# Kernel optimization log

Measured on AMD Instinct MI355X. Metric: run time of the kernel, lower is better.

Reference implementation:

```python
import jax, jax.numpy as jnp
import numpy as np
from jax import lax

T, B, F = 512, 256, 258
IN, H = 256, 1024


def setup_inputs() -> dict:
    key = jax.random.key(0)
    ks = jax.random.split(key, 6)

    def lin_w(k, fi, fo):
        return jax.random.normal(k, (fi, fo), jnp.float32) * (1.0 / np.sqrt(fi))

    return {
        "u": jax.random.normal(ks[0], (T, B, F), jnp.float32),
        "a": jnp.float32(0.92),
        "b": jnp.float32(-0.3),
        "W0": lin_w(ks[1], IN, H), "b0": jnp.zeros((H,), jnp.float32),
        "W1": lin_w(ks[2], H, H), "b1": jnp.zeros((H,), jnp.float32),
        "W2": lin_w(ks[3], H, H), "b2": jnp.zeros((H,), jnp.float32),
        "W3": lin_w(ks[4], H, 1), "b3": jnp.zeros((1,), jnp.float32),
    }


def reference(u, a, b, W0, b0, W1, b1, W2, b2, W3, b3):
    Tn, Bn, Fn = u.shape
    # MLP over cols 2: — independent of the recurrent state, so batch all timesteps.
    feats = u[:, :, 2:].reshape(Tn * Bn, Fn - 2)
    h = jax.nn.relu(feats @ W0 + b0)
    h = jax.nn.relu(h @ W1 + b1)
    h = jax.nn.relu(h @ W2 + b2)
    net = (h @ W3 + b3).reshape(Tn, Bn)  # [T, B]

    c1 = u[:, :, 1]  # [T, B], multiplied by b each step
    y0 = u[0, :, 0]  # u_y[0]; also the col-0 value used at j=0

    def step(carry, xs):
        net_j, c1_j = xs
        y = a * carry + b * c1_j + net_j
        return y, y

    _, ys = lax.scan(step, y0, (net, c1))  # ys: [T, B] = u_y[1:]
    return jnp.concatenate([y0[None, :], ys], axis=0)  # [T+1, B]
```

## Files before the change

### kernel.cpp

```cpp
#include <hip/hip_runtime.h>
#include <hip/hip_fp16.h>

typedef _Float16 v8h __attribute__((ext_vector_type(8)));
typedef _Float16 v4h __attribute__((ext_vector_type(4)));
typedef float v4f __attribute__((ext_vector_type(4)));

#define T_DIM 512
#define B_DIM 256
#define F_DIM 258
#define IN_DIM 256
#define H_DIM 1024
#define M_ROWS (T_DIM * B_DIM)

__device__ __forceinline__ void tile_map(int b, int nM, int nN, int& mt, int& nt) {
    if ((nM & 7) == 0) {
        int xcd = b & 7;
        int l = b >> 3;
        int mpx = nM >> 3;
        int lm = l / nN;
        mt = xcd * mpx + lm;
        nt = l - lm * nN;
    } else {
        int lm = b / nN;
        mt = lm;
        nt = b - lm * nN;
    }
}

__device__ __forceinline__ void gl16(const _Float16* g, _Float16* l) {
    __builtin_amdgcn_global_load_lds(
        (const __attribute__((address_space(1))) unsigned int*)g,
        (__attribute__((address_space(3))) unsigned int*)l, 16, 0, 0);
}


__global__ void prep_u_kernel(const float* __restrict__ u,
                              _Float16* __restrict__ X,
                              float* __restrict__ c1, int n) {
    int i = blockIdx.x * blockDim.x + threadIdx.x;
    int stride = gridDim.x * blockDim.x;
    for (; i < n; i += stride) {
        float v = u[i];
        unsigned r = (unsigned)i / 258u;
        unsigned c = (unsigned)i - r * 258u;
        if (c >= 2u) {
            unsigned k = c - 2u;
            X[((r >> 4) * 32u + (k >> 3)) * 128u + (r & 15u) * 8u + (k & 7u)] =
                (_Float16)v;
        } else if (c == 1u) {
            c1[r] = v;
        }
    }
}

__global__ void wt_frag_kernel(const float* __restrict__ W,
                               _Float16* __restrict__ BF, int K, int N) {
    int idx = blockIdx.x * blockDim.x + threadIdx.x;
    int total = (N >> 6) * (K >> 5) * 4 * 64;
    if (idx >= total) return;
    int l = idx & 63;
    int f = idx >> 6;
    int i = f & 3;
    int gk = f >> 2;
    int KC = K >> 5;
    int g = gk / KC, kc = gk - g * KC;
    int col = g * 64 + i * 16 + (l & 15);
    int krow = kc * 32 + (l >> 4) * 8;
    _Float16 tmp[8];
#pragma unroll
    for (int j = 0; j < 8; ++j) tmp[j] = (_Float16)W[(size_t)(krow + j) * N + col];
    *(v8h*)&BF[(size_t)idx * 8] = *(v8h*)tmp;
}

__global__ void wt_vec_kernel(const float* __restrict__ W,
                              _Float16* __restrict__ Wh, int K) {
    int i = blockIdx.x * blockDim.x + threadIdx.x;
    if (i < K) Wh[i] = (_Float16)W[i];
}

__global__ void zero_kernel(float* __restrict__ p, int n) {
    int i = blockIdx.x * blockDim.x + threadIdx.x;
    if (i < n) p[i] = 0.f;
}

template <int MI0>
__device__ __forceinline__ void mfma_pair(v4f (&acc)[8][4], const v8h (&af)[4][2],
                                          const v8h (&b)[4]) {
#pragma unroll
    for (int ni = 0; ni < 4; ++ni) {
        acc[MI0][ni] = __builtin_amdgcn_mfma_f32_16x16x32_f16(
            af[ni][0], b[0], acc[MI0][ni], 0, 0, 0);
        acc[MI0][ni] = __builtin_amdgcn_mfma_f32_16x16x32_f16(
            af[ni][1], b[1], acc[MI0][ni], 0, 0, 0);
        acc[MI0 + 1][ni] = __builtin_amdgcn_mfma_f32_16x16x32_f16(
            af[ni][0], b[2], acc[MI0 + 1][ni], 0, 0, 0);
        acc[MI0 + 1][ni] = __builtin_amdgcn_mfma_f32_16x16x32_f16(
            af[ni][1], b[3], acc[MI0 + 1][ni], 0, 0, 0);
    }
}

template <int DOT>
__global__ __launch_bounds__(512, 2)
void gemm256(const _Float16* __restrict__ Xb, const _Float16* __restrict__ WF,
             const float* __restrict__ bias, const _Float16* __restrict__ w3,
             _Float16* __restrict__ Cb, float* __restrict__ net,
             int M, int N, int K) {
    extern __shared__ _Float16 lds[];
    const int tid = threadIdx.x;
    const int lane = tid & 63;
    const int wave = tid >> 6;
    const int wm = wave >> 2;
    const int wn = wave & 3;
    const int quad = lane >> 4;
    const int r16 = lane & 15;
    const int wm8 = wm * 8;
    const int lrb = lane * 8;

    int mt, nt;
    tile_map(blockIdx.x, M >> 8, N >> 8, mt, nt);
    const int m0 = mt * 256;
    const int n0 = nt * 256;

    const int KC = K >> 5;
    const int KC8 = K >> 3;
    const int NT = K >> 6;
    const int m016 = m0 >> 4;
    const int nt4 = nt * 4;

    auto stageB = [&](int mb, int kt, _Float16* pb) {
        gl16(Xb + ((size_t)(m016 + mb + (tid >> 7)) * KC8 + (size_t)kt * 8) * 128 +
                 (tid & 127) * 8,
             pb + mb * 1024 + tid * 8);
    };
    auto loadB = [&](const _Float16* pB, int mb, v8h (&b)[4]) {
        b[0] = *(const v8h*)(pB + mb * 1024 + lrb);
        b[1] = *(const v8h*)(pB + mb * 1024 + 512 + lrb);
        b[2] = *(const v8h*)(pB + (mb + 1) * 1024 + lrb);
        b[3] = *(const v8h*)(pB + (mb + 1) * 1024 + 512 + lrb);
    };

    const _Float16* wp0 = WF + (size_t)(nt4 + wn) * KC * 2048 + lane * 8;

    v4f acc[8][4];
#pragma unroll
    for (int i = 0; i < 8; ++i)
#pragma unroll
        for (int j = 0; j < 4; ++j) acc[i][j] = (v4f)0.f;

    {
        stageB(0, 0, lds); stageB(4, 0, lds);
        stageB(8, 0, lds); stageB(12, 0, lds);
        asm volatile("s_waitcnt vmcnt(0)" ::: "memory");
        __builtin_amdgcn_s_barrier();
    }

#pragma unroll 2
    for (int kt = 0; kt < NT; ++kt) {
        _Float16* pBc = lds + (kt & 1) * 16384;
        _Float16* pBn = lds + ((kt + 1) & 1) * 16384;
        const bool pre = (kt + 1 < NT);
        const int kn = kt + 1;

        const _Float16* wpt = wp0 + (size_t)kt * 4096;
        v8h af[4][2];
#pragma unroll
        for (int i = 0; i < 4; ++i) {
            af[i][0] = *(const v8h*)(wpt + i * 512);
            af[i][1] = *(const v8h*)(wpt + 2048 + i * 512);
        }
        v8h bA[4], bB[4];
        loadB(pBc, wm8 + 0, bA);

        if (pre) {
            stageB(0, kn, pBn); stageB(4, kn, pBn);
            stageB(8, kn, pBn); stageB(12, kn, pBn);
        }

        loadB(pBc, wm8 + 2, bB);
        __builtin_amdgcn_s_setprio(1);
        mfma_pair<0>(acc, af, bA);
        __builtin_amdgcn_s_setprio(0);

        loadB(pBc, wm8 + 4, bA);
        __builtin_amdgcn_s_setprio(1);
        mfma_pair<2>(acc, af, bB);
        __builtin_amdgcn_s_setprio(0);

        loadB(pBc, wm8 + 6, bB);
        __builtin_amdgcn_s_setprio(1);
        mfma_pair<4>(acc, af, bA);
        __builtin_amdgcn_s_setprio(0);

        __builtin_amdgcn_s_setprio(1);
        mfma_pair<6>(acc, af, bB);
        __builtin_amdgcn_s_setprio(0);

        if (kt != NT - 1) {
            asm volatile("s_waitcnt lgkmcnt(0)" ::: "memory");
            asm volatile("s_waitcnt vmcnt(0)" ::: "memory");
            __builtin_amdgcn_s_barrier();
        }
    }

    const int nb = n0 + wn * 64;
    v4f bv[4];
#pragma unroll
    for (int ni = 0; ni < 4; ++ni)
        bv[ni] = *(const v4f*)&bias[nb + ni * 16 + quad * 4];

    if constexpr (DOT == 0) {
        const int NC8 = N >> 3;
#pragma unroll
        for (int ni = 0; ni < 4; ++ni) {
            const int nblk = ((nb + ni * 16) >> 3) + (quad >> 1);
#pragma unroll
            for (int mi = 0; mi < 8; ++mi) {
                v4h hv;
#pragma unroll
                for (int i = 0; i < 4; ++i)
                    hv[i] = (_Float16)fmaxf(acc[mi][ni][i] + bv[ni][i], 0.f);
                const size_t mblk = (size_t)((m0 + wm * 128 + mi * 16) >> 4);
                _Float16* dst =
                    Cb + (mblk * NC8 + nblk) * 128 + r16 * 8 + (quad & 1) * 4;
                *(v4h*)dst = hv;
            }
        }
    } else {
        v4h wv[4];
#pragma unroll
        for (int ni = 0; ni < 4; ++ni)
            wv[ni] = *(const v4h*)&w3[nb + ni * 16 + quad * 4];
#pragma unroll
        for (int mi = 0; mi < 8; ++mi) {
            float t = 0.f;
#pragma unroll
            for (int ni = 0; ni < 4; ++ni)
#pragma unroll
                for (int i = 0; i < 4; ++i) {
                    float v = fmaxf(acc[mi][ni][i] + bv[ni][i], 0.f);
                    t = fmaf(v, (float)wv[ni][i], t);
                }
            t += __shfl_xor(t, 16);
            t += __shfl_xor(t, 32);
            if (quad == 0) {
                int row = m0 + wm * 128 + mi * 16 + r16;
                atomicAdd(&net[row], t);
            }
        }
    }
}

__global__ void scan_kernel(const float* __restrict__ net,
                            const float* __restrict__ c1,
                            const float* __restrict__ u,
                            const float* __restrict__ pa,
                            const float* __restrict__ pb,
                            const float* __restrict__ pb3,
                            float* __restrict__ out) {
    const int bidx = threadIdx.x;
    const float a = pa[0];
    const float b = pb[0];
    const float b3 = pb3[0];
    float y = u[(size_t)bidx * F_DIM];
    out[bidx] = y;
#pragma unroll 8
    for (int t = 0; t < T_DIM; ++t) {
        float z = fmaf(b, c1[t * B_DIM + bidx], net[t * B_DIM + bidx] + b3);
        y = fmaf(a, y, z);
        out[(t + 1) * B_DIM + bidx] = y;
    }
}

extern "C" void kernel_launch(void* const* d_in, const int* in_sizes, int n_in,
                              void* d_out, int out_size, void* d_ws, size_t ws_size,
                              hipStream_t stream) {
    const float* u = (const float*)d_in[0];
    const float* pa = (const float*)d_in[1];
    const float* pb = (const float*)d_in[2];
    const float* W0 = (const float*)d_in[3];
    const float* b0 = (const float*)d_in[4];
    const float* W1 = (const float*)d_in[5];
    const float* b1 = (const float*)d_in[6];
    const float* W2 = (const float*)d_in[7];
    const float* b2 = (const float*)d_in[8];
    const float* W3 = (const float*)d_in[9];
    const float* b3 = (const float*)d_in[10];
    float* out = (float*)d_out;

    char* ws = (char*)d_ws;
    size_t off = 0;
    auto alloc = [&](size_t bytes) -> void* {
        void* p = ws + off;
        off += (bytes + 255) & ~(size_t)255;
        return p;
    };

    float* net = (float*)alloc((size_t)M_ROWS * 4);
    float* c1 = (float*)alloc((size_t)M_ROWS * 4);
    _Float16* W0F = (_Float16*)alloc((size_t)IN_DIM * H_DIM * 2);
    _Float16* W1F = (_Float16*)alloc((size_t)H_DIM * H_DIM * 2);
    _Float16* W2F = (_Float16*)alloc((size_t)H_DIM * H_DIM * 2);
    _Float16* W3h = (_Float16*)alloc((size_t)H_DIM * 2);

    const size_t per_row = 512 + 2048 + 2048;
    size_t avail = (ws_size > off + 65536) ? (ws_size - off - 65536) : 0;
    long Rl = (long)(avail / per_row);
    Rl = (Rl / 2048) * 2048;
    if (Rl < 2048) Rl = 2048;
    if (Rl > M_ROWS) Rl = M_ROWS;
    const int R = (int)Rl;

    _Float16* Xc = (_Float16*)alloc((size_t)R * IN_DIM * 2);
    _Float16* HAc = (_Float16*)alloc((size_t)R * H_DIM * 2);
    _Float16* HBc = (_Float16*)alloc((size_t)R * H_DIM * 2);

    wt_frag_kernel<<<(IN_DIM / 32) * (H_DIM / 64), 256, 0, stream>>>(W0, W0F,
                                                                     IN_DIM, H_DIM);
    wt_frag_kernel<<<(H_DIM / 32) * (H_DIM / 64), 256, 0, stream>>>(W1, W1F,
                                                                    H_DIM, H_DIM);
    wt_frag_kernel<<<(H_DIM / 32) * (H_DIM / 64), 256, 0, stream>>>(W2, W2F,
                                                                    H_DIM, H_DIM);
    wt_vec_kernel<<<4, 256, 0, stream>>>(W3, W3h, H_DIM);
    zero_kernel<<<M_ROWS / 256, 256, 0, stream>>>(net, M_ROWS);

    const size_t lds_bytes = 65536;
    for (int r0 = 0; r0 < M_ROWS; r0 += R) {
        int Mc = M_ROWS - r0;
        if (Mc > R) Mc = R;
        int nElem = Mc * F_DIM;
        int pgrid = (nElem + 256 * 8 - 1) / (256 * 8);
        if (pgrid > 2048) pgrid = 2048;
        prep_u_kernel<<<pgrid, 256, 0, stream>>>(u + (size_t)r0 * F_DIM, Xc,
                                                 c1 + r0, nElem);

        dim3 blk(512);
        dim3 grd((Mc / 256) * (H_DIM / 256));
        gemm256<0><<<grd, blk, lds_bytes, stream>>>(Xc, W0F, b0, nullptr, HAc,
                                                    nullptr, Mc, H_DIM, IN_DIM);
        gemm256<0><<<grd, blk, lds_bytes, stream>>>(HAc, W1F, b1, nullptr, HBc,
                                                    nullptr, Mc, H_DIM, H_DIM);
        gemm256<1><<<grd, blk, lds_bytes, stream>>>(HBc, W2F, b2, W3h, nullptr,
                                                    net + r0, Mc, H_DIM, H_DIM);
    }

    scan_kernel<<<1, 256, 0, stream>>>(net, c1, u, pa, pb, b3, out);
}
```

Baseline: 1.024 ms.

## Retile MLP GEMMs to 256x128 with LDS-staged weights and vectorize input prep

The GEMM block changes from 512 threads on a 256x256 tile with a 64-wide K step to 256 threads on a 256x128 tile with a 32-wide K step. Weight fragments are now staged into double-buffered LDS with global_load_lds instead of being read per wave straight from global memory, and LDS use drops to 48KB. The input prep kernel is split so the X conversion runs as 8-wide vectorized loads and stores without per-element division, while c1 gets its own small kernel. The smaller tile lowers arithmetic intensity and needs twice as many barriers per unit of K, in exchange for more blocks and less duplicated weight traffic.

```diff
diff --git a/kernel.cpp b/kernel.cpp
--- a/kernel.cpp
+++ b/kernel.cpp
@@ -34,23 +34,27 @@
 }
 
 
-__global__ void prep_u_kernel(const float* __restrict__ u,
-                              _Float16* __restrict__ X,
-                              float* __restrict__ c1, int n) {
+__global__ void prep_x_kernel(const float* __restrict__ u,
+                              _Float16* __restrict__ X, int nrows) {
     int i = blockIdx.x * blockDim.x + threadIdx.x;
+    int total = nrows * 32;
     int stride = gridDim.x * blockDim.x;
-    for (; i < n; i += stride) {
-        float v = u[i];
-        unsigned r = (unsigned)i / 258u;
-        unsigned c = (unsigned)i - r * 258u;
-        if (c >= 2u) {
-            unsigned k = c - 2u;
-            X[((r >> 4) * 32u + (k >> 3)) * 128u + (r & 15u) * 8u + (k & 7u)] =
-                (_Float16)v;
-        } else if (c == 1u) {
-            c1[r] = v;
-        }
-    }
+    for (; i < total; i += stride) {
+        int r = ((i >> 9) << 4) + (i & 15);
+        int kb = (i >> 4) & 31;
+        const float* s = u + (size_t)r * 258 + 2 + kb * 8;
+        _Float16 h[8];
+#pragma unroll
+        for (int j = 0; j < 8; ++j) h[j] = (_Float16)s[j];
+        *(v8h*)(X + ((size_t)(r >> 4) * 32 + kb) * 128 + (r & 15) * 8) =
+            *(v8h*)h;
+    }
+}
+
+__global__ void prep_c1_kernel(const float* __restrict__ u,
+                               float* __restrict__ c1, int nrows) {
+    int r = blockIdx.x * blockDim.x + threadIdx.x;
+    if (r < nrows) c1[r] = u[(size_t)r * 258 + 1];
 }
 
 __global__ void wt_frag_kernel(const float* __restrict__ W,
@@ -84,23 +88,18 @@
 }
 
 template <int MI0>
-__device__ __forceinline__ void mfma_pair(v4f (&acc)[8][4], const v8h (&af)[4][2],
-                                          const v8h (&b)[4]) {
-#pragma unroll
-    for (int ni = 0; ni < 4; ++ni) {
-        acc[MI0][ni] = __builtin_amdgcn_mfma_f32_16x16x32_f16(
-            af[ni][0], b[0], acc[MI0][ni], 0, 0, 0);
-        acc[MI0][ni] = __builtin_amdgcn_mfma_f32_16x16x32_f16(
-            af[ni][1], b[1], acc[MI0][ni], 0, 0, 0);
-        acc[MI0 + 1][ni] = __builtin_amdgcn_mfma_f32_16x16x32_f16(
-            af[ni][0], b[2], acc[MI0 + 1][ni], 0, 0, 0);
-        acc[MI0 + 1][ni] = __builtin_amdgcn_mfma_f32_16x16x32_f16(
-            af[ni][1], b[3], acc[MI0 + 1][ni], 0, 0, 0);
-    }
+__device__ __forceinline__ void mfma16(v4f (&acc)[8][4], const v8h (&af)[4],
+                                       const v8h (&b)[4]) {
+#pragma unroll
+    for (int mi = 0; mi < 4; ++mi)
+#pragma unroll
+        for (int ni = 0; ni < 4; ++ni)
+            acc[MI0 + mi][ni] = __builtin_amdgcn_mfma_f32_16x16x32_f16(
+                af[ni], b[mi], acc[MI0 + mi][ni], 0, 0, 0);
 }
 
 template <int DOT>
-__global__ __launch_bounds__(512, 2)
+__global__ __launch_bounds__(256, 2)
 void gemm256(const _Float16* __restrict__ Xb, const _Float16* __restrict__ WF,
              const float* __restrict__ bias, const _Float16* __restrict__ w3,
              _Float16* __restrict__ Cb, float* __restrict__ net,
@@ -109,38 +108,39 @@
     const int tid = threadIdx.x;
     const int lane = tid & 63;
     const int wave = tid >> 6;
-    const int wm = wave >> 2;
-    const int wn = wave & 3;
+    const int wm = wave >> 1;
+    const int wn = wave & 1;
     const int quad = lane >> 4;
     const int r16 = lane & 15;
     const int wm8 = wm * 8;
     const int lrb = lane * 8;
 
     int mt, nt;
-    tile_map(blockIdx.x, M >> 8, N >> 8, mt, nt);
+    tile_map(blockIdx.x, M >> 8, N >> 7, mt, nt);
     const int m0 = mt * 256;
-    const int n0 = nt * 256;
+    const int n0 = nt * 128;
 
     const int KC = K >> 5;
     const int KC8 = K >> 3;
-    const int NT = K >> 6;
+    const int NT = KC;
     const int m016 = m0 >> 4;
-    const int nt4 = nt * 4;
-
+    const int nt2 = nt * 2;
+
+    auto stageA = [&](int g, int kt, _Float16* pa) {
+        gl16(WF + ((size_t)(nt2 + g) * KC + kt) * 2048 + tid * 8,
+             pa + g * 2048 + tid * 8);
+    };
     auto stageB = [&](int mb, int kt, _Float16* pb) {
-        gl16(Xb + ((size_t)(m016 + mb + (tid >> 7)) * KC8 + (size_t)kt * 8) * 128 +
-                 (tid & 127) * 8,
-             pb + mb * 1024 + tid * 8);
+        gl16(Xb + ((size_t)(m016 + mb + (tid >> 6)) * KC8 + (size_t)kt * 4) * 128 +
+                 (tid & 63) * 8,
+             pb + mb * 512 + tid * 8);
     };
-    auto loadB = [&](const _Float16* pB, int mb, v8h (&b)[4]) {
-        b[0] = *(const v8h*)(pB + mb * 1024 + lrb);
-        b[1] = *(const v8h*)(pB + mb * 1024 + 512 + lrb);
-        b[2] = *(const v8h*)(pB + (mb + 1) * 1024 + lrb);
-        b[3] = *(const v8h*)(pB + (mb + 1) * 1024 + 512 + lrb);
+    auto loadB4 = [&](const _Float16* pB, int mb, v8h (&b)[4]) {
+#pragma unroll
+        for (int j = 0; j < 4; ++j)
+            b[j] = *(const v8h*)(pB + (mb + j) * 512 + lrb);
     };
 
-    const _Float16* wp0 = WF + (size_t)(nt4 + wn) * KC * 2048 + lane * 8;
-
     v4f acc[8][4];
 #pragma unroll
     for (int i = 0; i < 8; ++i)
@@ -148,55 +148,46 @@
         for (int j = 0; j < 4; ++j) acc[i][j] = (v4f)0.f;
 
     {
-        stageB(0, 0, lds); stageB(4, 0, lds);
-        stageB(8, 0, lds); stageB(12, 0, lds);
+        _Float16* A0 = lds;
+        _Float16* B0 = lds + 4096;
+        stageB(0, 0, B0); stageB(4, 0, B0); stageB(8, 0, B0); stageB(12, 0, B0);
+        stageA(0, 0, A0); stageA(1, 0, A0);
         asm volatile("s_waitcnt vmcnt(0)" ::: "memory");
         __builtin_amdgcn_s_barrier();
     }
 
 #pragma unroll 2
     for (int kt = 0; kt < NT; ++kt) {
-        _Float16* pBc = lds + (kt & 1) * 16384;
-        _Float16* pBn = lds + ((kt + 1) & 1) * 16384;
+        _Float16* pAc = lds + (kt & 1) * 12288;
+        _Float16* pBc = pAc + 4096;
+        _Float16* pAn = lds + ((kt + 1) & 1) * 12288;
+        _Float16* pBn = pAn + 4096;
         const bool pre = (kt + 1 < NT);
         const int kn = kt + 1;
 
-        const _Float16* wpt = wp0 + (size_t)kt * 4096;
-        v8h af[4][2];
-#pragma unroll
-        for (int i = 0; i < 4; ++i) {
-            af[i][0] = *(const v8h*)(wpt + i * 512);
-            af[i][1] = *(const v8h*)(wpt + 2048 + i * 512);
-        }
+        v8h af[4];
+#pragma unroll
+        for (int i = 0; i < 4; ++i)
+            af[i] = *(const v8h*)(pAc + wn * 2048 + i * 512 + lrb);
         v8h bA[4], bB[4];
-        loadB(pBc, wm8 + 0, bA);
+        loadB4(pBc, wm8 + 0, bA);
 
         if (pre) {
             stageB(0, kn, pBn); stageB(4, kn, pBn);
             stageB(8, kn, pBn); stageB(12, kn, pBn);
+            stageA(0, kn, pAn); stageA(1, kn, pAn);
         }
 
-        loadB(pBc, wm8 + 2, bB);
+        loadB4(pBc, wm8 + 4, bB);
+
         __builtin_amdgcn_s_setprio(1);
-        mfma_pair<0>(acc, af, bA);
+        mfma16<0>(acc, af, bA);
         __builtin_amdgcn_s_setprio(0);
-
-        loadB(pBc, wm8 + 4, bA);
         __builtin_amdgcn_s_setprio(1);
-        mfma_pair<2>(acc, af, bB);
+        mfma16<4>(acc, af, bB);
         __builtin_amdgcn_s_setprio(0);
 
-        loadB(pBc, wm8 + 6, bB);
-        __builtin_amdgcn_s_setprio(1);
-        mfma_pair<4>(acc, af, bA);
-        __builtin_amdgcn_s_setprio(0);
-
-        __builtin_amdgcn_s_setprio(1);
-        mfma_pair<6>(acc, af, bB);
-        __builtin_amdgcn_s_setprio(0);
-
         if (kt != NT - 1) {
-            asm volatile("s_waitcnt lgkmcnt(0)" ::: "memory");
             asm volatile("s_waitcnt vmcnt(0)" ::: "memory");
             __builtin_amdgcn_s_barrier();
         }
@@ -323,18 +314,19 @@
     wt_vec_kernel<<<4, 256, 0, stream>>>(W3, W3h, H_DIM);
     zero_kernel<<<M_ROWS / 256, 256, 0, stream>>>(net, M_ROWS);
 
-    const size_t lds_bytes = 65536;
+    const size_t lds_bytes = 49152;
     for (int r0 = 0; r0 < M_ROWS; r0 += R) {
         int Mc = M_ROWS - r0;
         if (Mc > R) Mc = R;
-        int nElem = Mc * F_DIM;
-        int pgrid = (nElem + 256 * 8 - 1) / (256 * 8);
+
+        int pgrid = (Mc * 32 + 255) / 256;
         if (pgrid > 2048) pgrid = 2048;
-        prep_u_kernel<<<pgrid, 256, 0, stream>>>(u + (size_t)r0 * F_DIM, Xc,
-                                                 c1 + r0, nElem);
-
-        dim3 blk(512);
-        dim3 grd((Mc / 256) * (H_DIM / 256));
+        prep_x_kernel<<<pgrid, 256, 0, stream>>>(u + (size_t)r0 * F_DIM, Xc, Mc);
+        prep_c1_kernel<<<(Mc + 255) / 256, 256, 0, stream>>>(
+            u + (size_t)r0 * F_DIM, c1 + r0, Mc);
+
+        dim3 blk(256);
+        dim3 grd((Mc / 256) * (H_DIM / 128));
         gemm256<0><<<grd, blk, lds_bytes, stream>>>(Xc, W0F, b0, nullptr, HAc,
                                                     nullptr, Mc, H_DIM, IN_DIM);
         gemm256<0><<<grd, blk, lds_bytes, stream>>>(HAc, W1F, b1, nullptr, HBc,
```

After: 926.5 us. 9.5% less time.
